# Kernel optimization log

Hardware: AMD Instinct MI355X
Metric: run time of the kernel (lower is better)

The kernel has to match this reference:

```python
import jax, jax.numpy as jnp
import numpy as np

T, H, D = 8192, 2048, 1024

def setup_inputs() -> dict:
    key = jax.random.key(0)
    k1, k2, k3 = jax.random.split(key, 3)
    x_sequence = jax.random.normal(k1, (T, D), dtype=jnp.float32)
    lamda = jax.random.normal(k2, (H,), dtype=jnp.float32) * 0.2
    B = jax.random.normal(k3, (H, D), dtype=jnp.float32) / jnp.sqrt(jnp.float32(D))
    return {"x_sequence": x_sequence, "lamda": lamda, "B": B}

def reference(x_sequence, lamda, B):
    # Batch all input projections into one GEMM: u[t] = B @ x[t]  -> [T, H]
    u = jnp.einsum('td,hd->th', x_sequence, B)
    a = jax.nn.sigmoid(lamda)  # [H], time-invariant diagonal decay

    def step(h, u_t):
        h = a * h + u_t
        return h, h

    h0 = jnp.zeros_like(lamda)
    _, outputs = jax.lax.scan(step, h0, u)  # [T, H]
    return outputs
```

## Files before the change

kernel.cpp:

```cpp
#include <hip/hip_runtime.h>
#include <hip/hip_bf16.h>

#define T_DIM 8192
#define H_DIM 2048
#define D_DIM 1024

typedef __bf16 bf16x8 __attribute__((ext_vector_type(8)));
typedef float floatx4 __attribute__((ext_vector_type(4)));
typedef unsigned short u16;

__device__ __forceinline__ u16 f2bf(float f) {
    __hip_bfloat16 b = __float2bfloat16(f);
    return *reinterpret_cast<u16*>(&b);
}
__device__ __forceinline__ float bf2f(u16 v) {
    return __uint_as_float((unsigned)v << 16);
}

__global__ __launch_bounds__(256) void f2bf2_kernel(const float* __restrict__ s0,
                                                    u16* __restrict__ d0, int n0_4,
                                                    const float* __restrict__ s1,
                                                    u16* __restrict__ d1, int n1_4) {
    int i = blockIdx.x * 256 + threadIdx.x;
    const float* s; u16* d;
    if (i < n0_4) { s = s0; d = d0; }
    else          { i -= n0_4; if (i >= n1_4) return; s = s1; d = d1; }
    const float4 v = reinterpret_cast<const float4*>(s)[i];
    ushort4 o;
    o.x = f2bf(v.x); o.y = f2bf(v.y); o.z = f2bf(v.z); o.w = f2bf(v.w);
    reinterpret_cast<ushort4*>(d)[i] = o;
}

#define GLDS(g, l) \
    __builtin_amdgcn_global_load_lds((const __attribute__((address_space(1))) void*)(g), \
                                     (__attribute__((address_space(3))) void*)(l), 16, 0, 0)

__global__ __launch_bounds__(256) void gemm_kernel(const u16* __restrict__ xb,
                                                   const u16* __restrict__ bb,
                                                   u16* __restrict__ u) {
    __shared__ alignas(16) u16 sA[128 * 64];
    __shared__ alignas(16) u16 sB[128 * 64];

    const int tid  = threadIdx.x;
    const int lane = tid & 63;
    const int wid  = tid >> 6;
    const int m0   = blockIdx.y * 128;
    const int n0   = blockIdx.x * 128;
    const int wm   = (wid >> 1) * 64;
    const int wn   = (wid & 1) * 64;
    const int lrow = lane & 15;
    const int kseg = lane >> 4;

    floatx4 acc[4][4] = {};

    const int r_s  = tid >> 3;
    const int cp_s = (tid & 7) * 8;

    const bf16x8* pA = reinterpret_cast<const bf16x8*>(sA);
    const bf16x8* pB = reinterpret_cast<const bf16x8*>(sB);

    for (int k0 = 0; k0 < D_DIM; k0 += 64) {
#pragma unroll
        for (int q = 0; q < 4; ++q) {
            const int r  = q * 32 + r_s;
            const int cg = cp_s ^ ((r & 7) * 8);
            GLDS(xb + (size_t)(m0 + r) * D_DIM + k0 + cg, &sA[q * 2048 + tid * 8]);
            GLDS(bb + (size_t)(n0 + r) * D_DIM + k0 + cg, &sB[q * 2048 + tid * 8]);
        }
        __syncthreads();

#pragma unroll
        for (int kk = 0; kk < 64; kk += 32) {
            bf16x8 af[4], bf[4];
#pragma unroll
            for (int i = 0; i < 4; ++i) {
                const int row = wm + i * 16 + lrow;
                const int cp  = (kk + kseg * 8) ^ ((row & 7) * 8);
                af[i] = pA[(row * 64 + cp) >> 3];
            }
#pragma unroll
            for (int j = 0; j < 4; ++j) {
                const int row = wn + j * 16 + lrow;
                const int cp  = (kk + kseg * 8) ^ ((row & 7) * 8);
                bf[j] = pB[(row * 64 + cp) >> 3];
            }
#pragma unroll
            for (int i = 0; i < 4; ++i)
#pragma unroll
                for (int j = 0; j < 4; ++j)
                    acc[i][j] = __builtin_amdgcn_mfma_f32_16x16x32_bf16(af[i], bf[j], acc[i][j], 0, 0, 0);
        }
        __syncthreads();
    }

#pragma unroll
    for (int i = 0; i < 4; ++i) {
#pragma unroll
        for (int j = 0; j < 4; ++j) {
            const int col = n0 + wn + j * 16 + lrow;
#pragma unroll
            for (int r = 0; r < 4; ++r) {
                const int row = m0 + wm + i * 16 + kseg * 4 + r;
                u[(size_t)row * H_DIM + col] = f2bf(acc[i][j][r]);
            }
        }
    }
}

__global__ __launch_bounds__(256) void scan_kernel(const u16* __restrict__ u,
                                                   const float* __restrict__ lam,
                                                   float* __restrict__ out,
                                                   int tl_begin, int gbase) {
    const int h   = blockIdx.y * 256 + threadIdx.x;
    const int tl0 = tl_begin + blockIdx.x * 64;

    const float a = 1.0f / (1.0f + __expf(-lam[h]));
    float hs = 0.0f;

    int ts = tl0 - 32;
    if (ts < 0) ts = 0;
#pragma unroll 8
    for (int t = ts; t < tl0; ++t)
        hs = fmaf(a, hs, bf2f(u[(size_t)t * H_DIM + h]));
#pragma unroll 8
    for (int t = tl0; t < tl0 + 64; ++t) {
        hs = fmaf(a, hs, bf2f(u[(size_t)t * H_DIM + h]));
        out[(size_t)(gbase + t) * H_DIM + h] = hs;
    }
}

extern "C" void kernel_launch(void* const* d_in, const int* in_sizes, int n_in,
                              void* d_out, int out_size, void* d_ws, size_t ws_size,
                              hipStream_t stream) {
    const float* x   = (const float*)d_in[0];
    const float* lam = (const float*)d_in[1];
    const float* B   = (const float*)d_in[2];
    float* out = (float*)d_out;

    int R = T_DIM;
    while (R > 128) {
        size_t need = (size_t)H_DIM * D_DIM * 2 +
                      (size_t)(R + 128) * (D_DIM + H_DIM) * 2;
        if (need <= ws_size) break;
        R >>= 1;
    }

    u16* bb = (u16*)d_ws;
    u16* xb = bb + (size_t)H_DIM * D_DIM;
    u16* u  = xb + (size_t)(R + 128) * D_DIM;

    const int nB4 = (H_DIM * D_DIM) / 4;

    for (int t_begin = 0; t_begin < T_DIM; t_begin += R) {
        const int base = (t_begin == 0) ? 0 : t_begin - 128;
        const int rows = t_begin + R - base;
        const int nX4  = (rows * D_DIM) / 4;
        f2bf2_kernel<<<(nB4 + nX4 + 255) / 256, 256, 0, stream>>>(
            B, bb, nB4, x + (size_t)base * D_DIM, xb, nX4);
        gemm_kernel<<<dim3(H_DIM / 128, rows / 128), 256, 0, stream>>>(xb, bb, u);
        scan_kernel<<<dim3(R / 64, H_DIM / 256), 256, 0, stream>>>(
            u, lam, out, t_begin - base, base);
    }
}
```

Measured before the change: 156.0 us.

## Fuse GEMM and scan into one kernel with overlapping time tiles

The GEMM and the scan now run in a single kernel. Each block computes a 160-row tile made of 128 output rows plus 32 zero-padded warm-up rows, stages the bf16 projections in shared memory, and then scans them in place. This removes the global round-trip of the intermediate u tensor and the chunking across separate launches. In exchange it recomputes 25% extra GEMM rows for the warm-up, and only 128 of the 256 threads run the serial scan, which leaves the other half idle during that phase.

Result: faster. 149.6 us (-4.1%).

```diff
diff --git a/kernel.cpp b/kernel.cpp
--- a/kernel.cpp
+++ b/kernel.cpp
@@ -4,6 +4,11 @@
 #define T_DIM 8192
 #define H_DIM 2048
 #define D_DIM 1024
+#define PAD_R 32
+#define MT    160
+#define NT    128
+#define BK    64
+#define USTR  132
 
 typedef __bf16 bf16x8 __attribute__((ext_vector_type(8)));
 typedef float floatx4 __attribute__((ext_vector_type(4)));
@@ -17,75 +22,94 @@
     return __uint_as_float((unsigned)v << 16);
 }
 
-__global__ __launch_bounds__(256) void f2bf2_kernel(const float* __restrict__ s0,
-                                                    u16* __restrict__ d0, int n0_4,
-                                                    const float* __restrict__ s1,
-                                                    u16* __restrict__ d1, int n1_4) {
+__global__ __launch_bounds__(256) void conv_kernel(const float* __restrict__ x,
+                                                   const float* __restrict__ Bm,
+                                                   u16* __restrict__ xb,
+                                                   u16* __restrict__ bb) {
+    const int nPad4 = PAD_R * D_DIM / 4;
+    const int nX4   = (T_DIM + PAD_R) * D_DIM / 4;
+    const int nB4   = H_DIM * D_DIM / 4;
     int i = blockIdx.x * 256 + threadIdx.x;
-    const float* s; u16* d;
-    if (i < n0_4) { s = s0; d = d0; }
-    else          { i -= n0_4; if (i >= n1_4) return; s = s1; d = d1; }
-    const float4 v = reinterpret_cast<const float4*>(s)[i];
-    ushort4 o;
-    o.x = f2bf(v.x); o.y = f2bf(v.y); o.z = f2bf(v.z); o.w = f2bf(v.w);
-    reinterpret_cast<ushort4*>(d)[i] = o;
+    if (i < nX4) {
+        ushort4 o;
+        if (i < nPad4) {
+            o.x = o.y = o.z = o.w = 0;
+        } else {
+            const float4 v = reinterpret_cast<const float4*>(x)[i - nPad4];
+            o.x = f2bf(v.x); o.y = f2bf(v.y); o.z = f2bf(v.z); o.w = f2bf(v.w);
+        }
+        reinterpret_cast<ushort4*>(xb)[i] = o;
+    } else {
+        i -= nX4;
+        if (i >= nB4) return;
+        const float4 v = reinterpret_cast<const float4*>(Bm)[i];
+        ushort4 o;
+        o.x = f2bf(v.x); o.y = f2bf(v.y); o.z = f2bf(v.z); o.w = f2bf(v.w);
+        reinterpret_cast<ushort4*>(bb)[i] = o;
+    }
 }
 
 #define GLDS(g, l) \
     __builtin_amdgcn_global_load_lds((const __attribute__((address_space(1))) void*)(g), \
                                      (__attribute__((address_space(3))) void*)(l), 16, 0, 0)
 
-__global__ __launch_bounds__(256) void gemm_kernel(const u16* __restrict__ xb,
-                                                   const u16* __restrict__ bb,
-                                                   u16* __restrict__ u) {
-    __shared__ alignas(16) u16 sA[128 * 64];
-    __shared__ alignas(16) u16 sB[128 * 64];
+__global__ __launch_bounds__(256) void fused_kernel(const u16* __restrict__ xb,
+                                                    const u16* __restrict__ bb,
+                                                    const float* __restrict__ lam,
+                                                    float* __restrict__ out) {
+    __shared__ alignas(16) u16 smem[MT * USTR];
+    u16* sA = smem;
+    u16* sB = smem + MT * BK;
+    u16* us = smem;
 
     const int tid  = threadIdx.x;
     const int lane = tid & 63;
     const int wid  = tid >> 6;
-    const int m0   = blockIdx.y * 128;
+    const int pm0  = blockIdx.y * 128;
     const int n0   = blockIdx.x * 128;
-    const int wm   = (wid >> 1) * 64;
+    const int wm   = (wid >> 1) * 80;
     const int wn   = (wid & 1) * 64;
     const int lrow = lane & 15;
     const int kseg = lane >> 4;
 
-    floatx4 acc[4][4] = {};
+    floatx4 acc[5][4] = {};
 
-    const int r_s  = tid >> 3;
-    const int cp_s = (tid & 7) * 8;
+    const int r_s = tid >> 3;
+    const int cg  = ((tid & 7) * 8) ^ ((r_s & 7) * 8);
+
+    const u16* gA = xb + (size_t)(pm0 + r_s) * D_DIM + cg;
+    const u16* gB = bb + (size_t)(n0 + r_s) * D_DIM + cg;
 
     const bf16x8* pA = reinterpret_cast<const bf16x8*>(sA);
     const bf16x8* pB = reinterpret_cast<const bf16x8*>(sB);
 
-    for (int k0 = 0; k0 < D_DIM; k0 += 64) {
+    for (int it = 0; it < D_DIM / BK; ++it) {
 #pragma unroll
-        for (int q = 0; q < 4; ++q) {
-            const int r  = q * 32 + r_s;
-            const int cg = cp_s ^ ((r & 7) * 8);
-            GLDS(xb + (size_t)(m0 + r) * D_DIM + k0 + cg, &sA[q * 2048 + tid * 8]);
-            GLDS(bb + (size_t)(n0 + r) * D_DIM + k0 + cg, &sB[q * 2048 + tid * 8]);
-        }
+        for (int q = 0; q < 5; ++q)
+            GLDS(gA + (size_t)(q * 32) * D_DIM, &sA[q * 2048 + tid * 8]);
+#pragma unroll
+        for (int q = 0; q < 4; ++q)
+            GLDS(gB + (size_t)(q * 32) * D_DIM, &sB[q * 2048 + tid * 8]);
+        gA += BK; gB += BK;
         __syncthreads();
 
 #pragma unroll
-        for (int kk = 0; kk < 64; kk += 32) {
-            bf16x8 af[4], bf[4];
+        for (int kk = 0; kk < BK; kk += 32) {
+            bf16x8 af[5], bf[4];
 #pragma unroll
-            for (int i = 0; i < 4; ++i) {
+            for (int i = 0; i < 5; ++i) {
                 const int row = wm + i * 16 + lrow;
                 const int cp  = (kk + kseg * 8) ^ ((row & 7) * 8);
-                af[i] = pA[(row * 64 + cp) >> 3];
+                af[i] = pA[(row * BK + cp) >> 3];
             }
 #pragma unroll
             for (int j = 0; j < 4; ++j) {
                 const int row = wn + j * 16 + lrow;
                 const int cp  = (kk + kseg * 8) ^ ((row & 7) * 8);
-                bf[j] = pB[(row * 64 + cp) >> 3];
+                bf[j] = pB[(row * BK + cp) >> 3];
             }
 #pragma unroll
-            for (int i = 0; i < 4; ++i)
+            for (int i = 0; i < 5; ++i)
 #pragma unroll
                 for (int j = 0; j < 4; ++j)
                     acc[i][j] = __builtin_amdgcn_mfma_f32_16x16x32_bf16(af[i], bf[j], acc[i][j], 0, 0, 0);
@@ -94,38 +118,32 @@
     }
 
 #pragma unroll
-    for (int i = 0; i < 4; ++i) {
+    for (int i = 0; i < 5; ++i) {
 #pragma unroll
         for (int j = 0; j < 4; ++j) {
-            const int col = n0 + wn + j * 16 + lrow;
+            const int col = wn + j * 16 + lrow;
 #pragma unroll
             for (int r = 0; r < 4; ++r) {
-                const int row = m0 + wm + i * 16 + kseg * 4 + r;
-                u[(size_t)row * H_DIM + col] = f2bf(acc[i][j][r]);
+                const int row = wm + i * 16 + kseg * 4 + r;
+                us[row * USTR + col] = f2bf(acc[i][j][r]);
             }
         }
     }
-}
+    __syncthreads();
 
-__global__ __launch_bounds__(256) void scan_kernel(const u16* __restrict__ u,
-                                                   const float* __restrict__ lam,
-                                                   float* __restrict__ out,
-                                                   int tl_begin, int gbase) {
-    const int h   = blockIdx.y * 256 + threadIdx.x;
-    const int tl0 = tl_begin + blockIdx.x * 64;
-
-    const float a = 1.0f / (1.0f + __expf(-lam[h]));
-    float hs = 0.0f;
-
-    int ts = tl0 - 32;
-    if (ts < 0) ts = 0;
+    if (tid < 128) {
+        const int h  = n0 + tid;
+        const float a = 1.0f / (1.0f + __expf(-lam[h]));
+        float hs = 0.0f;
+        float* op = out + (size_t)(blockIdx.y * 128) * H_DIM + h;
 #pragma unroll 8
-    for (int t = ts; t < tl0; ++t)
-        hs = fmaf(a, hs, bf2f(u[(size_t)t * H_DIM + h]));
+        for (int tl = 0; tl < PAD_R; ++tl)
+            hs = fmaf(a, hs, bf2f(us[tl * USTR + tid]));
 #pragma unroll 8
-    for (int t = tl0; t < tl0 + 64; ++t) {
-        hs = fmaf(a, hs, bf2f(u[(size_t)t * H_DIM + h]));
-        out[(size_t)(gbase + t) * H_DIM + h] = hs;
+        for (int tl = PAD_R; tl < MT; ++tl) {
+            hs = fmaf(a, hs, bf2f(us[tl * USTR + tid]));
+            op[(size_t)(tl - PAD_R) * H_DIM] = hs;
+        }
     }
 }
 
@@ -137,28 +155,10 @@
     const float* B   = (const float*)d_in[2];
     float* out = (float*)d_out;
 
-    int R = T_DIM;
-    while (R > 128) {
-        size_t need = (size_t)H_DIM * D_DIM * 2 +
-                      (size_t)(R + 128) * (D_DIM + H_DIM) * 2;
-        if (need <= ws_size) break;
-        R >>= 1;
-    }
+    u16* xb = (u16*)d_ws;
+    u16* bb = xb + (size_t)(T_DIM + PAD_R) * D_DIM;
 
-    u16* bb = (u16*)d_ws;
-    u16* xb = bb + (size_t)H_DIM * D_DIM;
-    u16* u  = xb + (size_t)(R + 128) * D_DIM;
-
-    const int nB4 = (H_DIM * D_DIM) / 4;
-
-    for (int t_begin = 0; t_begin < T_DIM; t_begin += R) {
-        const int base = (t_begin == 0) ? 0 : t_begin - 128;
-        const int rows = t_begin + R - base;
-        const int nX4  = (rows * D_DIM) / 4;
-        f2bf2_kernel<<<(nB4 + nX4 + 255) / 256, 256, 0, stream>>>(
-            B, bb, nB4, x + (size_t)base * D_DIM, xb, nX4);
-        gemm_kernel<<<dim3(H_DIM / 128, rows / 128), 256, 0, stream>>>(xb, bb, u);
-        scan_kernel<<<dim3(R / 64, H_DIM / 256), 256, 0, stream>>>(
-            u, lam, out, t_begin - base, base);
-    }
+    const int n4 = ((T_DIM + PAD_R) * D_DIM + H_DIM * D_DIM) / 4;
+    conv_kernel<<<(n4 + 255) / 256, 256, 0, stream>>>(x, B, xb, bb);
+    fused_kernel<<<dim3(H_DIM / 128, T_DIM / 128), 256, 0, stream>>>(xb, bb, lam, out);
 }
```
